# Optimization experiments

Measured on AMD Instinct MI355X. Metric: run time of the kernel, lower is better.

Reference implementation:

```python
import jax, jax.numpy as jnp
import numpy as np

IGNORE = 255


def interp_bilinear_ac(x, H, W):
    """Bilinear interpolation with align_corners=True. x: [B,C,h,w] -> [B,C,H,W]."""
    B, C, h, w = x.shape

    def coords(n_in, n_out):
        s = jnp.linspace(0.0, n_in - 1.0, n_out)
        i0 = jnp.clip(jnp.floor(s).astype(jnp.int32), 0, n_in - 2)
        t = (s - i0).astype(x.dtype)
        return i0, t

    y0, ty = coords(h, H)
    x = x[:, :, y0, :] * (1.0 - ty)[None, None, :, None] + x[:, :, y0 + 1, :] * ty[None, None, :, None]
    x0, tx = coords(w, W)
    x = x[:, :, :, x0] * (1.0 - tx) + x[:, :, :, x0 + 1] * tx
    return x


def cross_entropy(logits, labels):
    """Mean CE over valid pixels. logits: [B,C,H,W], labels: [B,H,W] int."""
    C = logits.shape[1]
    logp = jax.nn.log_softmax(logits, axis=1)
    lab = jnp.clip(labels, 0, C - 1)
    nll = -jnp.take_along_axis(logp, lab[:, None], axis=1)[:, 0]  # [B,H,W]
    valid = (labels != IGNORE).astype(logits.dtype)
    return jnp.sum(nll * valid) / jnp.maximum(jnp.sum(valid), 1.0)


def lovasz_softmax_flat(probs_flat, labels_flat, valid):
    """Multi-class Lovasz-Softmax, only_present=True. probs_flat: [P,C], labels_flat: [P]."""
    P, C = probs_flat.shape
    classes = jnp.arange(C)
    fg = ((labels_flat[None, :] == classes[:, None]) & valid[None, :]).astype(probs_flat.dtype)  # [C,P]
    vf = jnp.broadcast_to(valid, (C, P)).astype(probs_flat.dtype)
    # invalid pixels get error -1 so descending sort puts them last
    errors = jnp.where(valid[None, :], jnp.abs(fg - probs_flat.T), -1.0)
    order = jnp.argsort(-errors, axis=1)
    err_s = jnp.take_along_axis(errors, order, axis=1)
    fg_s = jnp.take_along_axis(fg, order, axis=1)
    val_s = jnp.take_along_axis(vf, order, axis=1)
    gts = jnp.sum(fg_s, axis=1, keepdims=True)
    inter = gts - jnp.cumsum(fg_s, axis=1)
    union = gts + jnp.cumsum(val_s - fg_s, axis=1)
    jac = 1.0 - inter / jnp.maximum(union, 1.0)
    jac = jnp.concatenate([jac[:, :1], jac[:, 1:] - jac[:, :-1]], axis=1)
    per_class = jnp.sum(jnp.where(val_s > 0, err_s, 0.0) * jax.lax.stop_gradient(jac), axis=1)
    present = gts[:, 0] > 0
    n = jnp.maximum(jnp.sum(present.astype(probs_flat.dtype)), 1.0)
    return jnp.sum(jnp.where(present, per_class, 0.0)) / n


def lovasz_branch(logits, labels, H, W):
    p = jax.nn.softmax(interp_bilinear_ac(logits, H, W), axis=1)
    C = p.shape[1]
    probs_flat = jnp.transpose(p, (0, 2, 3, 1)).reshape(-1, C)
    labels_flat = labels.reshape(-1)
    return lovasz_softmax_flat(probs_flat, labels_flat, labels_flat != IGNORE)


def setup_inputs() -> dict:
    key = jax.random.key(0)
    ks = jax.random.split(key, 7)
    B, hs, ws, H, W = 4, 96, 96, 384, 384
    return {
        "preds0": jax.random.normal(ks[0], (B, 7, hs, ws), dtype=jnp.float32),
        "preds1": jax.random.normal(ks[1], (B, 3, hs, ws), dtype=jnp.float32),
        "preds2": jax.random.normal(ks[2], (B, 2, hs, ws), dtype=jnp.float32),
        "preds_dsn": jax.random.normal(ks[3], (B, 7, hs, ws), dtype=jnp.float32),
        "targets0": jax.random.randint(ks[4], (B, H, W), 0, 7, dtype=jnp.int32),
        "targets1": jax.random.randint(ks[5], (B, H, W), 0, 3, dtype=jnp.int32),
        "targets2": jax.random.randint(ks[6], (B, H, W), 0, 2, dtype=jnp.int32),
    }


def reference(preds0, preds1, preds2, preds_dsn, targets0, targets1, targets2):
    H, W = targets0.shape[1], targets0.shape[2]
    pred = interp_bilinear_ac(preds0, H, W)
    loss_ce = cross_entropy(pred, targets0)
    probs = jax.nn.softmax(pred, axis=1)
    C = probs.shape[1]
    probs_flat = jnp.transpose(probs, (0, 2, 3, 1)).reshape(-1, C)
    labels_flat = targets0.reshape(-1)
    loss = lovasz_softmax_flat(probs_flat, labels_flat, labels_flat != IGNORE)
    loss_hb = lovasz_branch(preds1, targets1, H, W)
    loss_fb = lovasz_branch(preds2, targets2, H, W)
    pred_dsn = interp_bilinear_ac(preds_dsn, H, W)
    loss_dsn = cross_entropy(pred_dsn, targets0)
    return loss_ce + loss + 0.4 * loss_hb + 0.4 * loss_fb + 0.4 * loss_dsn
```

## Files before the change

kernel.cpp:

```cpp
#include <hip/hip_runtime.h>

#define NBUCK 64
#define NCLS 12
#define NCHUNK 16
#define NBMAIN 576
#define SPC (NBMAIN / NCHUNK)
#define SUBH 4
#define HSTRIDE (NCLS*NBUCK + 8)
#define IGNORE_LBL 255
#define PIX (4*384*384)

typedef float float4a __attribute__((ext_vector_type(4), aligned(4)));


__global__ __launch_bounds__(512) void k_main(
    const float* __restrict__ p0, const float* __restrict__ p1,
    const float* __restrict__ p2, const float* __restrict__ pdsn,
    const int* __restrict__ t0, const int* __restrict__ t1, const int* __restrict__ t2,
    unsigned int* __restrict__ slices, float4* __restrict__ ce_part)
{
    __shared__ unsigned int h[SUBH * HSTRIDE];
    __shared__ float cw[8][3];
    int t = threadIdx.x;
    for (int i = t; i < SUBH * HSTRIDE; i += 512) h[i] = 0u;
    __syncthreads();

    int role = t >> 8;
    int lt = t & 255;
    int sub = t & 3;
    unsigned int* hs = h + sub * HSTRIDE;
    int g = blockIdx.x * 256 + lt;
    int gx = g % 96;
    int row = g / 96;
    int y = row % 384;
    int b = row / 384;
    int x4 = gx * 4;

    const float scale = 95.0f / 383.0f;
    float sy = y * scale;
    int y0 = (int)sy; if (y0 > 94) y0 = 94;
    float ty = sy - (float)y0;
    float oty = 1.0f - ty;
    float sx0 = (float)x4 * scale;
    int X0 = (int)sx0; if (X0 > 92) X0 = 92;

    float Wa[4][4], Wb[4][4];
    #pragma unroll
    for (int i = 0; i < 4; i++) {
        float sx = (float)(x4 + i) * scale;
        #pragma unroll
        for (int j = 0; j < 4; j++) {
            float w = fmaxf(1.0f - fabsf(sx - (float)(X0 + j)), 0.0f);
            Wa[i][j] = w * oty;
            Wb[i][j] = w * ty;
        }
    }

    const int rb = y0 * 96 + X0;

    auto interp4 = [&](const float* A, int c, float zout[4]) {
        float4a r0 = *(const float4a*)(A + c * 9216);
        float4a r1 = *(const float4a*)(A + c * 9216 + 96);
        #pragma unroll
        for (int i = 0; i < 4; i++) {
            zout[i] = r0.x*Wa[i][0] + r0.y*Wa[i][1] + r0.z*Wa[i][2] + r0.w*Wa[i][3]
                    + r1.x*Wb[i][0] + r1.y*Wb[i][1] + r1.z*Wb[i][2] + r1.w*Wb[i][3];
        }
    };
    auto histadd = [&](int cls, int fg, float err) {
        int bk = (int)(err * (float)NBUCK);
        if (bk > NBUCK - 1) bk = NBUCK - 1;
        atomicAdd(&hs[cls * NBUCK + bk], 0x10000u | (unsigned)fg);
    };

    float nll = 0.f, nll2 = 0.f; int vc = 0;

    int4 L0 = *(const int4*)(t0 + g * 4);
    int l0v[4] = {L0.x, L0.y, L0.z, L0.w};

    if (role == 0) {
        const float* A0 = p0 + b * 7 * 9216 + rb;
        float z0[7][4];
        #pragma unroll
        for (int c = 0; c < 7; c++) interp4(A0, c, z0[c]);
        #pragma unroll
        for (int i = 0; i < 4; i++) {
            int l = l0v[i];
            if (l != IGNORE_LBL) {
                float e[7]; e[0] = 1.0f; float s = 1.0f;
                #pragma unroll
                for (int c = 1; c < 7; c++) { e[c] = __expf(z0[c][i] - z0[0][i]); s += e[c]; }
                float inv = 1.0f / s;
                float zl = z0[0][i];
                #pragma unroll
                for (int c = 1; c < 7; c++) zl = (l == c) ? z0[c][i] : zl;
                nll += __logf(s) - (zl - z0[0][i]);
                vc++;
                #pragma unroll
                for (int c = 0; c < 7; c++) {
                    int fg = (l == c);
                    histadd(c, fg, fabsf((float)fg - e[c] * inv));
                }
            }
        }
    } else {
        const float* Ad = pdsn + b * 7 * 9216 + rb;
        float zd[7][4];
        #pragma unroll
        for (int c = 0; c < 7; c++) interp4(Ad, c, zd[c]);
        #pragma unroll
        for (int i = 0; i < 4; i++) {
            int l = l0v[i];
            if (l != IGNORE_LBL) {
                float s = 1.0f;
                #pragma unroll
                for (int c = 1; c < 7; c++) s += __expf(zd[c][i] - zd[0][i]);
                float zl = zd[0][i];
                #pragma unroll
                for (int c = 1; c < 7; c++) zl = (l == c) ? zd[c][i] : zl;
                nll2 += __logf(s) - (zl - zd[0][i]);
            }
        }

        int4 L1 = *(const int4*)(t1 + g * 4);
        int l1v[4] = {L1.x, L1.y, L1.z, L1.w};

        const float* A1 = p1 + b * 3 * 9216 + rb;
        float z1[3][4];
        #pragma unroll
        for (int c = 0; c < 3; c++) interp4(A1, c, z1[c]);
        #pragma unroll
        for (int i = 0; i < 4; i++) {
            int l = l1v[i];
            if (l != IGNORE_LBL) {
                float e1 = __expf(z1[1][i] - z1[0][i]);
                float e2 = __expf(z1[2][i] - z1[0][i]);
                float inv = 1.0f / (1.0f + e1 + e2);
                histadd(7 + 0, (l == 0), fabsf((float)(l == 0) - inv));
                histadd(7 + 1, (l == 1), fabsf((float)(l == 1) - e1 * inv));
                histadd(7 + 2, (l == 2), fabsf((float)(l == 2) - e2 * inv));
            }
        }

        int4 L2 = *(const int4*)(t2 + g * 4);
        int l2v[4] = {L2.x, L2.y, L2.z, L2.w};

        const float* A2 = p2 + b * 2 * 9216 + rb;
        float z2a[2][4];
        #pragma unroll
        for (int c = 0; c < 2; c++) interp4(A2, c, z2a[c]);
        #pragma unroll
        for (int i = 0; i < 4; i++) {
            int l = l2v[i];
            if (l != IGNORE_LBL) {
                float p0c = 1.0f / (1.0f + __expf(z2a[1][i] - z2a[0][i]));
                histadd(10, (l == 0), fabsf((float)(l == 0) - p0c));
            }
        }
    }

    #pragma unroll
    for (int o = 32; o > 0; o >>= 1) {
        nll  += __shfl_down(nll, o);
        nll2 += __shfl_down(nll2, o);
        vc   += __shfl_down(vc, o);
    }
    int wv = t >> 6, ln = t & 63;
    if (ln == 0) { cw[wv][0] = nll; cw[wv][1] = nll2; cw[wv][2] = (float)vc; }
    __syncthreads();
    if (t == 0) {
        float a = 0.f, bb = 0.f, cc = 0.f;
        #pragma unroll
        for (int w = 0; w < 8; w++) { a += cw[w][0]; bb += cw[w][1]; cc += cw[w][2]; }
        ce_part[blockIdx.x] = make_float4(a, bb, cc, 0.f);
    }

    unsigned int* dst = slices + (size_t)blockIdx.x * (NCLS * NBUCK);
    for (int i = t; i < NCLS * NBUCK; i += 512)
        dst[i] = h[i] + h[HSTRIDE + i] + h[2 * HSTRIDE + i] + h[3 * HSTRIDE + i];
}

__global__ __launch_bounds__(64) void k_merge(
    const unsigned int* __restrict__ slices, unsigned int* __restrict__ partial)
{
    int kk = blockIdx.x % NCLS;
    int cy = blockIdx.x / NCLS;
    int bk = threadIdx.x;
    int s0 = cy * SPC;
    unsigned int acc = 0;
    for (int s = 0; s < SPC; s++)
        acc += slices[(size_t)((s0 + s) * NCLS + kk) * NBUCK + bk];
    partial[(size_t)(cy * NCLS + kk) * NBUCK + bk] = acc;
}

__global__ __launch_bounds__(512) void k_fin(
    const unsigned int* __restrict__ partial, const float4* __restrict__ ce_part,
    float* __restrict__ out)
{
    int t = threadIdx.x;
    __shared__ float ce_tot[3];
    __shared__ float cwf[8][3];
    __shared__ unsigned long long sc[512];
    __shared__ float sf[512];
    __shared__ float cls_lov[NCLS];
    __shared__ float cls_pres[NCLS];

    float a = 0.f, bb = 0.f, cc = 0.f;
    for (int e = t; e < NBMAIN; e += 512) {
        float4 v = ce_part[e];
        a += v.x; bb += v.y; cc += v.z;
    }
    #pragma unroll
    for (int o = 32; o > 0; o >>= 1) {
        a += __shfl_down(a, o); bb += __shfl_down(bb, o); cc += __shfl_down(cc, o);
    }
    if ((t & 63) == 0) { cwf[t >> 6][0] = a; cwf[t >> 6][1] = bb; cwf[t >> 6][2] = cc; }
    __syncthreads();
    if (t == 0) {
        float x = 0.f, y = 0.f, z = 0.f;
        for (int w = 0; w < 8; w++) { x += cwf[w][0]; y += cwf[w][1]; z += cwf[w][2]; }
        ce_tot[0] = x; ce_tot[1] = y; ce_tot[2] = z;
    }

    int sub = t >> 6;
    int p   = t & 63;
    int bk  = NBUCK - 1 - p;

    for (int r = 0; r < 2; r++) {
        int kk = r * 8 + sub;
        unsigned int cnt = 0, fg = 0;
        if (kk < NCLS) {
            int src = (kk == 11) ? 10 : kk;
            #pragma unroll
            for (int cy = 0; cy < NCHUNK; cy++) {
                unsigned int v = partial[(size_t)(cy * NCLS + src) * NBUCK + bk];
                cnt += v >> 16; fg += v & 0xffffu;
            }
            if (kk == 11) fg = cnt - fg;
        }
        unsigned long long own = ((unsigned long long)cnt << 32) | fg;
        __syncthreads();
        sc[t] = own;
        __syncthreads();
        #pragma unroll
        for (int o = 1; o < 64; o <<= 1) {
            unsigned long long add = (p >= o) ? sc[t - o] : 0ull;
            __syncthreads();
            sc[t] += add;
            __syncthreads();
        }
        unsigned long long total = sc[(sub << 6) + 63];
        unsigned long long excl = sc[t] - own;
        unsigned int G = (unsigned int)(total & 0xffffffffu);

        float contrib = 0.f;
        if (G > 0 && cnt > 0) {
            unsigned int rr = (unsigned int)(excl >> 32);
            unsigned int F  = (unsigned int)(excl & 0xffffffffu);
            float fG = (float)G;
            float j0 = 1.0f - (fG - (float)F) / fmaxf(fG + (float)rr - (float)F, 1.0f);
            rr += cnt; F += fg;
            float j1 = 1.0f - (fG - (float)F) / fmaxf(fG + (float)rr - (float)F, 1.0f);
            contrib = (((float)bk + 0.5f) * (1.0f / (float)NBUCK)) * (j1 - j0);
        }
        sf[t] = contrib;
        __syncthreads();
        #pragma unroll
        for (int o = 32; o > 0; o >>= 1) {
            if (p < o) sf[t] += sf[t + o];
            __syncthreads();
        }
        if (p == 0 && kk < NCLS) {
            cls_lov[kk]  = (G > 0) ? sf[t] : 0.f;
            cls_pres[kk] = (G > 0) ? 1.f : 0.f;
        }
    }
    __syncthreads();

    if (t == 0) {
        float l0 = 0.f, p0c = 0.f, l1 = 0.f, p1c = 0.f, l2 = 0.f, p2c = 0.f;
        for (int k = 0; k < 7;  k++) { l0 += cls_lov[k]; p0c += cls_pres[k]; }
        for (int k = 7; k < 10; k++) { l1 += cls_lov[k]; p1c += cls_pres[k]; }
        for (int k = 10; k < 12; k++) { l2 += cls_lov[k]; p2c += cls_pres[k]; }
        float vcnt = fmaxf(ce_tot[2], 1.0f);
        out[0] = ce_tot[0] / vcnt
               + l0 / fmaxf(p0c, 1.f)
               + 0.4f * (l1 / fmaxf(p1c, 1.f))
               + 0.4f * (l2 / fmaxf(p2c, 1.f))
               + 0.4f * (ce_tot[1] / vcnt);
    }
}

extern "C" void kernel_launch(void* const* d_in, const int* in_sizes, int n_in,
                              void* d_out, int out_size, void* d_ws, size_t ws_size,
                              hipStream_t stream)
{
    const float* p0 = (const float*)d_in[0];
    const float* p1 = (const float*)d_in[1];
    const float* p2 = (const float*)d_in[2];
    const float* pd = (const float*)d_in[3];
    const int* t0 = (const int*)d_in[4];
    const int* t1 = (const int*)d_in[5];
    const int* t2 = (const int*)d_in[6];

    char* ws = (char*)d_ws;
    const size_t partial_bytes = (size_t)NCHUNK * NCLS * NBUCK * 4;
    const size_t cepart_bytes = (size_t)NBMAIN * 16;
    unsigned int* partial = (unsigned int*)ws;
    float4* ce_part = (float4*)(ws + partial_bytes);
    unsigned int* slices = (unsigned int*)(ws + partial_bytes + cepart_bytes);

    k_main<<<NBMAIN, 512, 0, stream>>>(p0, p1, p2, pd, t0, t1, t2, slices, ce_part);
    k_merge<<<NCLS * NCHUNK, 64, 0, stream>>>(slices, partial);
    k_fin<<<1, 512, 0, stream>>>(partial, ce_part, (float*)d_out);
}
```

Baseline: 26.07 us.

## Fuse merge and finalize into main kernel via global atomics and last-block pattern

Drops the separate merge and finalize kernels. Each block now atomically adds its nonzero shared histogram bins into one of 16 global partial histograms, and its CE sums into 8 double-precision accumulators. The last block to finish, found with an atomic counter, runs the Lovasz finalization. The shared histogram is also reduced from four sub-copies to one, which increases LDS atomic contention. The change removes two kernel launches and the slice round-trip through memory, but adds a memset launch, global atomic traffic and a serialized tail on one block.

```diff
diff --git a/kernel.cpp b/kernel.cpp
--- a/kernel.cpp
+++ b/kernel.cpp
@@ -2,11 +2,9 @@
 
 #define NBUCK 64
 #define NCLS 12
-#define NCHUNK 16
 #define NBMAIN 576
-#define SPC (NBMAIN / NCHUNK)
-#define SUBH 4
-#define HSTRIDE (NCLS*NBUCK + 8)
+#define NPART 16
+#define NENT (NCLS*NBUCK)
 #define IGNORE_LBL 255
 #define PIX (4*384*384)
 
@@ -17,18 +15,18 @@
     const float* __restrict__ p0, const float* __restrict__ p1,
     const float* __restrict__ p2, const float* __restrict__ pdsn,
     const int* __restrict__ t0, const int* __restrict__ t1, const int* __restrict__ t2,
-    unsigned int* __restrict__ slices, float4* __restrict__ ce_part)
+    unsigned int* __restrict__ done, double* __restrict__ ce_acc,
+    unsigned int* __restrict__ pcnt, float* __restrict__ out)
 {
-    __shared__ unsigned int h[SUBH * HSTRIDE];
+    __shared__ unsigned int h[NENT];
     __shared__ float cw[8][3];
+    __shared__ unsigned int is_last;
     int t = threadIdx.x;
-    for (int i = t; i < SUBH * HSTRIDE; i += 512) h[i] = 0u;
+    for (int i = t; i < NENT; i += 512) h[i] = 0u;
     __syncthreads();
 
     int role = t >> 8;
     int lt = t & 255;
-    int sub = t & 3;
-    unsigned int* hs = h + sub * HSTRIDE;
     int g = blockIdx.x * 256 + lt;
     int gx = g % 96;
     int row = g / 96;
@@ -70,7 +68,7 @@
     auto histadd = [&](int cls, int fg, float err) {
         int bk = (int)(err * (float)NBUCK);
         if (bk > NBUCK - 1) bk = NBUCK - 1;
-        atomicAdd(&hs[cls * NBUCK + bk], 0x10000u | (unsigned)fg);
+        atomicAdd(&h[cls * NBUCK + bk], 0x10000u | (unsigned)fg);
     };
 
     float nll = 0.f, nll2 = 0.f; int vc = 0;
@@ -168,58 +166,44 @@
     int wv = t >> 6, ln = t & 63;
     if (ln == 0) { cw[wv][0] = nll; cw[wv][1] = nll2; cw[wv][2] = (float)vc; }
     __syncthreads();
+
     if (t == 0) {
         float a = 0.f, bb = 0.f, cc = 0.f;
         #pragma unroll
         for (int w = 0; w < 8; w++) { a += cw[w][0]; bb += cw[w][1]; cc += cw[w][2]; }
-        ce_part[blockIdx.x] = make_float4(a, bb, cc, 0.f);
-    }
-
-    unsigned int* dst = slices + (size_t)blockIdx.x * (NCLS * NBUCK);
-    for (int i = t; i < NCLS * NBUCK; i += 512)
-        dst[i] = h[i] + h[HSTRIDE + i] + h[2 * HSTRIDE + i] + h[3 * HSTRIDE + i];
-}
-
-__global__ __launch_bounds__(64) void k_merge(
-    const unsigned int* __restrict__ slices, unsigned int* __restrict__ partial)
-{
-    int kk = blockIdx.x % NCLS;
-    int cy = blockIdx.x / NCLS;
-    int bk = threadIdx.x;
-    int s0 = cy * SPC;
-    unsigned int acc = 0;
-    for (int s = 0; s < SPC; s++)
-        acc += slices[(size_t)((s0 + s) * NCLS + kk) * NBUCK + bk];
-    partial[(size_t)(cy * NCLS + kk) * NBUCK + bk] = acc;
-}
-
-__global__ __launch_bounds__(512) void k_fin(
-    const unsigned int* __restrict__ partial, const float4* __restrict__ ce_part,
-    float* __restrict__ out)
-{
-    int t = threadIdx.x;
+        double* ca = ce_acc + (blockIdx.x & 7) * 3;
+        atomicAdd(&ca[0], (double)a);
+        atomicAdd(&ca[1], (double)bb);
+        atomicAdd(&ca[2], (double)cc);
+    }
+
+    unsigned int* pp = pcnt + (size_t)(blockIdx.x & (NPART - 1)) * NENT;
+    for (int i = t; i < NENT; i += 512) {
+        unsigned int v = h[i];
+        if (v) atomicAdd(&pp[i], v);
+    }
+
+    __threadfence();
+    __syncthreads();
+    if (t == 0) is_last = (atomicAdd(done, 1u) == NBMAIN - 1) ? 1u : 0u;
+    __syncthreads();
+    if (!is_last) return;
+    __threadfence();
+
+    __shared__ double cef[24];
     __shared__ float ce_tot[3];
-    __shared__ float cwf[8][3];
     __shared__ unsigned long long sc[512];
     __shared__ float sf[512];
     __shared__ float cls_lov[NCLS];
     __shared__ float cls_pres[NCLS];
 
-    float a = 0.f, bb = 0.f, cc = 0.f;
-    for (int e = t; e < NBMAIN; e += 512) {
-        float4 v = ce_part[e];
-        a += v.x; bb += v.y; cc += v.z;
-    }
-    #pragma unroll
-    for (int o = 32; o > 0; o >>= 1) {
-        a += __shfl_down(a, o); bb += __shfl_down(bb, o); cc += __shfl_down(cc, o);
-    }
-    if ((t & 63) == 0) { cwf[t >> 6][0] = a; cwf[t >> 6][1] = bb; cwf[t >> 6][2] = cc; }
+    if (t < 24) cef[t] = atomicAdd(&ce_acc[t], 0.0);
     __syncthreads();
     if (t == 0) {
-        float x = 0.f, y = 0.f, z = 0.f;
-        for (int w = 0; w < 8; w++) { x += cwf[w][0]; y += cwf[w][1]; z += cwf[w][2]; }
-        ce_tot[0] = x; ce_tot[1] = y; ce_tot[2] = z;
+        double a = 0, bb = 0, cc = 0;
+        #pragma unroll
+        for (int w = 0; w < 8; w++) { a += cef[w*3]; bb += cef[w*3+1]; cc += cef[w*3+2]; }
+        ce_tot[0] = (float)a; ce_tot[1] = (float)bb; ce_tot[2] = (float)cc;
     }
 
     int sub = t >> 6;
@@ -232,8 +216,8 @@
         if (kk < NCLS) {
             int src = (kk == 11) ? 10 : kk;
             #pragma unroll
-            for (int cy = 0; cy < NCHUNK; cy++) {
-                unsigned int v = partial[(size_t)(cy * NCLS + src) * NBUCK + bk];
+            for (int cy = 0; cy < NPART; cy++) {
+                unsigned int v = atomicAdd(&pcnt[(size_t)cy * NENT + src * NBUCK + bk], 0u);
                 cnt += v >> 16; fg += v & 0xffffu;
             }
             if (kk == 11) fg = cnt - fg;
@@ -304,13 +288,12 @@
     const int* t2 = (const int*)d_in[6];
 
     char* ws = (char*)d_ws;
-    const size_t partial_bytes = (size_t)NCHUNK * NCLS * NBUCK * 4;
-    const size_t cepart_bytes = (size_t)NBMAIN * 16;
-    unsigned int* partial = (unsigned int*)ws;
-    float4* ce_part = (float4*)(ws + partial_bytes);
-    unsigned int* slices = (unsigned int*)(ws + partial_bytes + cepart_bytes);
-
-    k_main<<<NBMAIN, 512, 0, stream>>>(p0, p1, p2, pd, t0, t1, t2, slices, ce_part);
-    k_merge<<<NCLS * NCHUNK, 64, 0, stream>>>(slices, partial);
-    k_fin<<<1, 512, 0, stream>>>(partial, ce_part, (float*)d_out);
+    unsigned int* done = (unsigned int*)ws;
+    double* ce_acc = (double*)(ws + 16);
+    unsigned int* pcnt = (unsigned int*)(ws + 256);
+
+    hipMemsetAsync(d_ws, 0, 256 + (size_t)NPART * NENT * 4, stream);
+
+    k_main<<<NBMAIN, 512, 0, stream>>>(p0, p1, p2, pd, t0, t1, t2,
+                                       done, ce_acc, pcnt, (float*)d_out);
 }
```

New measurement: 90.59 us. 3.47x slower.

## Stage low-res logit rows in shared memory and drop sub-histogram replication

Applied to the files above, without the earlier changes.

Each block now cooperatively loads the few low-resolution source rows it needs for all 19 logit planes into shared memory with aligned vector loads, and the bilinear interpolation reads from LDS instead of issuing unaligned global loads per thread. The four replicated per-block histograms are merged into a single shared histogram, which cuts LDS footprint and the final reduction. In exchange, atomic contention on the single histogram rises and an extra staging pass with a barrier precedes compute.

```diff
diff --git a/kernel.cpp b/kernel.cpp
--- a/kernel.cpp
+++ b/kernel.cpp
@@ -5,12 +5,13 @@
 #define NCHUNK 16
 #define NBMAIN 576
 #define SPC (NBMAIN / NCHUNK)
-#define SUBH 4
-#define HSTRIDE (NCLS*NBUCK + 8)
+#define NPLANES 19
+#define SROWS 3
 #define IGNORE_LBL 255
 #define PIX (4*384*384)
 
-typedef float float4a __attribute__((ext_vector_type(4), aligned(4)));
+typedef float float4a  __attribute__((ext_vector_type(4), aligned(4)));
+typedef float float4al __attribute__((ext_vector_type(4), aligned(16)));
 
 
 __global__ __launch_bounds__(512) void k_main(
@@ -19,28 +20,49 @@
     const int* __restrict__ t0, const int* __restrict__ t1, const int* __restrict__ t2,
     unsigned int* __restrict__ slices, float4* __restrict__ ce_part)
 {
-    __shared__ unsigned int h[SUBH * HSTRIDE];
+    __shared__ float stage[NPLANES * SROWS * 96];
+    __shared__ unsigned int h[NCLS * NBUCK];
     __shared__ float cw[8][3];
     int t = threadIdx.x;
-    for (int i = t; i < SUBH * HSTRIDE; i += 512) h[i] = 0u;
+    for (int i = t; i < NCLS * NBUCK; i += 512) h[i] = 0u;
+
+    int g0 = blockIdx.x * 256;
+    int row0 = g0 / 96;
+    int ys = row0 % 384;
+    int b = row0 / 384;
+
+    const float scale = 95.0f / 383.0f;
+    int Y = (int)((float)ys * scale);
+
+    for (int q = t; q < NPLANES * SROWS * 24; q += 512) {
+        int p = q / (SROWS * 24);
+        int rem = q % (SROWS * 24);
+        int r = rem / 24;
+        int c4 = rem % 24;
+        int gy = Y + r; if (gy > 95) gy = 95;
+        const float* src;
+        if (p < 7)       src = p0   + (b * 7 + p)        * 9216;
+        else if (p < 14) src = pdsn + (b * 7 + (p - 7))  * 9216;
+        else if (p < 17) src = p1   + (b * 3 + (p - 14)) * 9216;
+        else             src = p2   + (b * 2 + (p - 17)) * 9216;
+        *(float4al*)&stage[(p * SROWS + r) * 96 + c4 * 4] =
+            *(const float4al*)(src + gy * 96 + c4 * 4);
+    }
     __syncthreads();
 
     int role = t >> 8;
     int lt = t & 255;
-    int sub = t & 3;
-    unsigned int* hs = h + sub * HSTRIDE;
-    int g = blockIdx.x * 256 + lt;
+    int g = g0 + lt;
     int gx = g % 96;
     int row = g / 96;
     int y = row % 384;
-    int b = row / 384;
     int x4 = gx * 4;
 
-    const float scale = 95.0f / 383.0f;
-    float sy = y * scale;
+    float sy = (float)y * scale;
     int y0 = (int)sy; if (y0 > 94) y0 = 94;
     float ty = sy - (float)y0;
     float oty = 1.0f - ty;
+    int ry = y0 - Y;
     float sx0 = (float)x4 * scale;
     int X0 = (int)sx0; if (X0 > 92) X0 = 92;
 
@@ -56,11 +78,12 @@
         }
     }
 
-    const int rb = y0 * 96 + X0;
-
-    auto interp4 = [&](const float* A, int c, float zout[4]) {
-        float4a r0 = *(const float4a*)(A + c * 9216);
-        float4a r1 = *(const float4a*)(A + c * 9216 + 96);
+    const int sb = ry * 96 + X0;
+
+    auto interp4 = [&](int plane, float zout[4]) {
+        const float* q = &stage[plane * (SROWS * 96) + sb];
+        float4a r0 = *(const float4a*)q;
+        float4a r1 = *(const float4a*)(q + 96);
         #pragma unroll
         for (int i = 0; i < 4; i++) {
             zout[i] = r0.x*Wa[i][0] + r0.y*Wa[i][1] + r0.z*Wa[i][2] + r0.w*Wa[i][3]
@@ -70,7 +93,7 @@
     auto histadd = [&](int cls, int fg, float err) {
         int bk = (int)(err * (float)NBUCK);
         if (bk > NBUCK - 1) bk = NBUCK - 1;
-        atomicAdd(&hs[cls * NBUCK + bk], 0x10000u | (unsigned)fg);
+        atomicAdd(&h[cls * NBUCK + bk], 0x10000u | (unsigned)fg);
     };
 
     float nll = 0.f, nll2 = 0.f; int vc = 0;
@@ -79,10 +102,9 @@
     int l0v[4] = {L0.x, L0.y, L0.z, L0.w};
 
     if (role == 0) {
-        const float* A0 = p0 + b * 7 * 9216 + rb;
         float z0[7][4];
         #pragma unroll
-        for (int c = 0; c < 7; c++) interp4(A0, c, z0[c]);
+        for (int c = 0; c < 7; c++) interp4(c, z0[c]);
         #pragma unroll
         for (int i = 0; i < 4; i++) {
             int l = l0v[i];
@@ -104,10 +126,9 @@
             }
         }
     } else {
-        const float* Ad = pdsn + b * 7 * 9216 + rb;
         float zd[7][4];
         #pragma unroll
-        for (int c = 0; c < 7; c++) interp4(Ad, c, zd[c]);
+        for (int c = 0; c < 7; c++) interp4(7 + c, zd[c]);
         #pragma unroll
         for (int i = 0; i < 4; i++) {
             int l = l0v[i];
@@ -125,10 +146,9 @@
         int4 L1 = *(const int4*)(t1 + g * 4);
         int l1v[4] = {L1.x, L1.y, L1.z, L1.w};
 
-        const float* A1 = p1 + b * 3 * 9216 + rb;
         float z1[3][4];
         #pragma unroll
-        for (int c = 0; c < 3; c++) interp4(A1, c, z1[c]);
+        for (int c = 0; c < 3; c++) interp4(14 + c, z1[c]);
         #pragma unroll
         for (int i = 0; i < 4; i++) {
             int l = l1v[i];
@@ -145,10 +165,9 @@
         int4 L2 = *(const int4*)(t2 + g * 4);
         int l2v[4] = {L2.x, L2.y, L2.z, L2.w};
 
-        const float* A2 = p2 + b * 2 * 9216 + rb;
         float z2a[2][4];
         #pragma unroll
-        for (int c = 0; c < 2; c++) interp4(A2, c, z2a[c]);
+        for (int c = 0; c < 2; c++) interp4(17 + c, z2a[c]);
         #pragma unroll
         for (int i = 0; i < 4; i++) {
             int l = l2v[i];
@@ -176,8 +195,7 @@
     }
 
     unsigned int* dst = slices + (size_t)blockIdx.x * (NCLS * NBUCK);
-    for (int i = t; i < NCLS * NBUCK; i += 512)
-        dst[i] = h[i] + h[HSTRIDE + i] + h[2 * HSTRIDE + i] + h[3 * HSTRIDE + i];
+    for (int i = t; i < NCLS * NBUCK; i += 512) dst[i] = h[i];
 }
 
 __global__ __launch_bounds__(64) void k_merge(
```

Result: slower. 27.13 us (+4.1%).

## Use one thread per pixel group for all branches with single histogram, 32 buckets

Applied to the files above, without the earlier changes.

Each thread now processes all four prediction branches for its four pixels, where before a 512-thread block split the work into two roles of 256 threads. Blocks become 128 threads and the grid doubles. The four replicated shared histograms are merged into one, and the bucket count drops from 64 to 32, which also shrinks the merge and finalize kernels. The intent is to cut block-level imbalance, shared-memory zeroing and slice traffic. In exchange it adds more shared-atomic contention on a single histogram, more registers per thread, and a coarser Lovasz approximation.

```diff
diff --git a/kernel.cpp b/kernel.cpp
--- a/kernel.cpp
+++ b/kernel.cpp
@@ -1,35 +1,31 @@
 #include <hip/hip_runtime.h>
 
-#define NBUCK 64
+#define NBUCK 32
 #define NCLS 12
 #define NCHUNK 16
-#define NBMAIN 576
+#define NBMAIN 1152
 #define SPC (NBMAIN / NCHUNK)
-#define SUBH 4
-#define HSTRIDE (NCLS*NBUCK + 8)
+#define NENT (NCLS * NBUCK)
 #define IGNORE_LBL 255
 #define PIX (4*384*384)
 
 typedef float float4a __attribute__((ext_vector_type(4), aligned(4)));
 
 
-__global__ __launch_bounds__(512) void k_main(
+__global__ __launch_bounds__(128) void k_main(
     const float* __restrict__ p0, const float* __restrict__ p1,
     const float* __restrict__ p2, const float* __restrict__ pdsn,
     const int* __restrict__ t0, const int* __restrict__ t1, const int* __restrict__ t2,
     unsigned int* __restrict__ slices, float4* __restrict__ ce_part)
 {
-    __shared__ unsigned int h[SUBH * HSTRIDE];
-    __shared__ float cw[8][3];
+    __shared__ unsigned int h[NENT];
+    __shared__ float cw[2][3];
     int t = threadIdx.x;
-    for (int i = t; i < SUBH * HSTRIDE; i += 512) h[i] = 0u;
-    __syncthreads();
-
-    int role = t >> 8;
-    int lt = t & 255;
-    int sub = t & 3;
-    unsigned int* hs = h + sub * HSTRIDE;
-    int g = blockIdx.x * 256 + lt;
+    #pragma unroll
+    for (int i = t; i < NENT; i += 128) h[i] = 0u;
+    __syncthreads();
+
+    int g = blockIdx.x * 128 + t;
     int gx = g % 96;
     int row = g / 96;
     int y = row % 384;
@@ -70,7 +66,7 @@
     auto histadd = [&](int cls, int fg, float err) {
         int bk = (int)(err * (float)NBUCK);
         if (bk > NBUCK - 1) bk = NBUCK - 1;
-        atomicAdd(&hs[cls * NBUCK + bk], 0x10000u | (unsigned)fg);
+        atomicAdd(&h[cls * NBUCK + bk], 0x10000u | (unsigned)fg);
     };
 
     float nll = 0.f, nll2 = 0.f; int vc = 0;
@@ -78,7 +74,7 @@
     int4 L0 = *(const int4*)(t0 + g * 4);
     int l0v[4] = {L0.x, L0.y, L0.z, L0.w};
 
-    if (role == 0) {
+    {
         const float* A0 = p0 + b * 7 * 9216 + rb;
         float z0[7][4];
         #pragma unroll
@@ -103,7 +99,9 @@
                 }
             }
         }
-    } else {
+    }
+
+    {
         const float* Ad = pdsn + b * 7 * 9216 + rb;
         float zd[7][4];
         #pragma unroll
@@ -121,10 +119,11 @@
                 nll2 += __logf(s) - (zl - zd[0][i]);
             }
         }
-
+    }
+
+    {
         int4 L1 = *(const int4*)(t1 + g * 4);
         int l1v[4] = {L1.x, L1.y, L1.z, L1.w};
-
         const float* A1 = p1 + b * 3 * 9216 + rb;
         float z1[3][4];
         #pragma unroll
@@ -141,10 +140,11 @@
                 histadd(7 + 2, (l == 2), fabsf((float)(l == 2) - e2 * inv));
             }
         }
-
+    }
+
+    {
         int4 L2 = *(const int4*)(t2 + g * 4);
         int l2v[4] = {L2.x, L2.y, L2.z, L2.w};
-
         const float* A2 = p2 + b * 2 * 9216 + rb;
         float z2a[2][4];
         #pragma unroll
@@ -169,18 +169,17 @@
     if (ln == 0) { cw[wv][0] = nll; cw[wv][1] = nll2; cw[wv][2] = (float)vc; }
     __syncthreads();
     if (t == 0) {
-        float a = 0.f, bb = 0.f, cc = 0.f;
-        #pragma unroll
-        for (int w = 0; w < 8; w++) { a += cw[w][0]; bb += cw[w][1]; cc += cw[w][2]; }
-        ce_part[blockIdx.x] = make_float4(a, bb, cc, 0.f);
-    }
-
-    unsigned int* dst = slices + (size_t)blockIdx.x * (NCLS * NBUCK);
-    for (int i = t; i < NCLS * NBUCK; i += 512)
-        dst[i] = h[i] + h[HSTRIDE + i] + h[2 * HSTRIDE + i] + h[3 * HSTRIDE + i];
+        ce_part[blockIdx.x] = make_float4(cw[0][0] + cw[1][0],
+                                          cw[0][1] + cw[1][1],
+                                          cw[0][2] + cw[1][2], 0.f);
+    }
+
+    unsigned int* dst = slices + (size_t)blockIdx.x * NENT;
+    #pragma unroll
+    for (int i = t; i < NENT; i += 128) dst[i] = h[i];
 }
 
-__global__ __launch_bounds__(64) void k_merge(
+__global__ __launch_bounds__(32) void k_merge(
     const unsigned int* __restrict__ slices, unsigned int* __restrict__ partial)
 {
     int kk = blockIdx.x % NCLS;
@@ -189,7 +188,7 @@
     int s0 = cy * SPC;
     unsigned int acc = 0;
     for (int s = 0; s < SPC; s++)
-        acc += slices[(size_t)((s0 + s) * NCLS + kk) * NBUCK + bk];
+        acc += slices[(size_t)(s0 + s) * NENT + kk * NBUCK + bk];
     partial[(size_t)(cy * NCLS + kk) * NBUCK + bk] = acc;
 }
 
@@ -222,58 +221,55 @@
         ce_tot[0] = x; ce_tot[1] = y; ce_tot[2] = z;
     }
 
-    int sub = t >> 6;
-    int p   = t & 63;
+    int sub = t >> 5;
+    int p   = t & 31;
     int bk  = NBUCK - 1 - p;
 
-    for (int r = 0; r < 2; r++) {
-        int kk = r * 8 + sub;
-        unsigned int cnt = 0, fg = 0;
-        if (kk < NCLS) {
-            int src = (kk == 11) ? 10 : kk;
-            #pragma unroll
-            for (int cy = 0; cy < NCHUNK; cy++) {
-                unsigned int v = partial[(size_t)(cy * NCLS + src) * NBUCK + bk];
-                cnt += v >> 16; fg += v & 0xffffu;
-            }
-            if (kk == 11) fg = cnt - fg;
-        }
-        unsigned long long own = ((unsigned long long)cnt << 32) | fg;
+    int kk = sub;
+    unsigned int cnt = 0, fg = 0;
+    if (kk < NCLS) {
+        int src = (kk == 11) ? 10 : kk;
+        #pragma unroll
+        for (int cy = 0; cy < NCHUNK; cy++) {
+            unsigned int v = partial[(size_t)(cy * NCLS + src) * NBUCK + bk];
+            cnt += v >> 16; fg += v & 0xffffu;
+        }
+        if (kk == 11) fg = cnt - fg;
+    }
+    unsigned long long own = ((unsigned long long)cnt << 32) | fg;
+    sc[t] = own;
+    __syncthreads();
+    #pragma unroll
+    for (int o = 1; o < 32; o <<= 1) {
+        unsigned long long add = (p >= o) ? sc[t - o] : 0ull;
         __syncthreads();
-        sc[t] = own;
+        sc[t] += add;
         __syncthreads();
-        #pragma unroll
-        for (int o = 1; o < 64; o <<= 1) {
-            unsigned long long add = (p >= o) ? sc[t - o] : 0ull;
-            __syncthreads();
-            sc[t] += add;
-            __syncthreads();
-        }
-        unsigned long long total = sc[(sub << 6) + 63];
-        unsigned long long excl = sc[t] - own;
-        unsigned int G = (unsigned int)(total & 0xffffffffu);
-
-        float contrib = 0.f;
-        if (G > 0 && cnt > 0) {
-            unsigned int rr = (unsigned int)(excl >> 32);
-            unsigned int F  = (unsigned int)(excl & 0xffffffffu);
-            float fG = (float)G;
-            float j0 = 1.0f - (fG - (float)F) / fmaxf(fG + (float)rr - (float)F, 1.0f);
-            rr += cnt; F += fg;
-            float j1 = 1.0f - (fG - (float)F) / fmaxf(fG + (float)rr - (float)F, 1.0f);
-            contrib = (((float)bk + 0.5f) * (1.0f / (float)NBUCK)) * (j1 - j0);
-        }
-        sf[t] = contrib;
+    }
+    unsigned long long total = sc[(sub << 5) + 31];
+    unsigned long long excl = sc[t] - own;
+    unsigned int G = (unsigned int)(total & 0xffffffffu);
+
+    float contrib = 0.f;
+    if (G > 0 && cnt > 0) {
+        unsigned int rr = (unsigned int)(excl >> 32);
+        unsigned int F  = (unsigned int)(excl & 0xffffffffu);
+        float fG = (float)G;
+        float j0 = 1.0f - (fG - (float)F) / fmaxf(fG + (float)rr - (float)F, 1.0f);
+        rr += cnt; F += fg;
+        float j1 = 1.0f - (fG - (float)F) / fmaxf(fG + (float)rr - (float)F, 1.0f);
+        contrib = (((float)bk + 0.5f) * (1.0f / (float)NBUCK)) * (j1 - j0);
+    }
+    sf[t] = contrib;
+    __syncthreads();
+    #pragma unroll
+    for (int o = 16; o > 0; o >>= 1) {
+        if (p < o) sf[t] += sf[t + o];
         __syncthreads();
-        #pragma unroll
-        for (int o = 32; o > 0; o >>= 1) {
-            if (p < o) sf[t] += sf[t + o];
-            __syncthreads();
-        }
-        if (p == 0 && kk < NCLS) {
-            cls_lov[kk]  = (G > 0) ? sf[t] : 0.f;
-            cls_pres[kk] = (G > 0) ? 1.f : 0.f;
-        }
+    }
+    if (p == 0 && kk < NCLS) {
+        cls_lov[kk]  = (G > 0) ? sf[t] : 0.f;
+        cls_pres[kk] = (G > 0) ? 1.f : 0.f;
     }
     __syncthreads();
 
@@ -304,13 +300,13 @@
     const int* t2 = (const int*)d_in[6];
 
     char* ws = (char*)d_ws;
-    const size_t partial_bytes = (size_t)NCHUNK * NCLS * NBUCK * 4;
+    const size_t partial_bytes = (size_t)NCHUNK * NENT * 4;
     const size_t cepart_bytes = (size_t)NBMAIN * 16;
     unsigned int* partial = (unsigned int*)ws;
     float4* ce_part = (float4*)(ws + partial_bytes);
     unsigned int* slices = (unsigned int*)(ws + partial_bytes + cepart_bytes);
 
-    k_main<<<NBMAIN, 512, 0, stream>>>(p0, p1, p2, pd, t0, t1, t2, slices, ce_part);
-    k_merge<<<NCLS * NCHUNK, 64, 0, stream>>>(slices, partial);
+    k_main<<<NBMAIN, 128, 0, stream>>>(p0, p1, p2, pd, t0, t1, t2, slices, ce_part);
+    k_merge<<<NCLS * NCHUNK, 32, 0, stream>>>(slices, partial);
     k_fin<<<1, 512, 0, stream>>>(partial, ce_part, (float*)d_out);
 }
```

Result: no change. 25.59 us (-1.8%).
